# Kernel tuning notes

Hardware: AMD Instinct MI355X
Metric: run time of the kernel (lower is better)

The kernel has to match this reference:

```python
import jax, jax.numpy as jnp
import numpy as np
from functools import partial

H = 512          # hidden_size
H4 = H // 4      # goal hidden size
ENC = 8          # enc_steps
DEC = 12         # dec_steps
PRED = 2         # pred_dim (ETH)
B = 512          # batch


def _lin(k, i, o, s=0.05):
    kw, kb = jax.random.split(k)
    return jax.random.normal(kw, (i, o), jnp.float32) * s, jax.random.normal(kb, (o,), jnp.float32) * s


def setup_inputs() -> dict:
    key = jax.random.key(0)
    ks = jax.random.split(key, 32)
    d = {"inputs": jax.random.normal(ks[0], (B, ENC, 6), jnp.float32)}
    d["embed_w"], d["embed_b"] = _lin(ks[1], 6, H)
    d["reg_w"], d["reg_b"] = _lin(ks[2], H, PRED)
    d["ea_w"], d["ea_b"] = _lin(ks[3], H4, 1)
    d["da_w"], d["da_b"] = _lin(ks[4], H4, 1)
    d["e2g_w"], d["e2g_b"] = _lin(ks[5], H, H4)
    d["e2d_w"], d["e2d_b"] = _lin(ks[6], H, H)
    d["gh2i_w"], d["gh2i_b"] = _lin(ks[7], H4, H4)
    d["dh2i_w"], d["dh2i_b"] = _lin(ks[8], H, H)
    d["gh2t_w"], d["gh2t_b"] = _lin(ks[9], H4, H)
    d["g2e_w"], d["g2e_b"] = _lin(ks[10], H4, H4)
    d["g2d_w"], d["g2d_b"] = _lin(ks[11], H4, H4)
    d["enc_wih"], _ = _lin(ks[12], H + H4, 3 * H)
    d["enc_whh"], _ = _lin(ks[13], H, 3 * H)
    d["enc_bih"] = jax.random.normal(ks[14], (3 * H,), jnp.float32) * 0.05
    d["enc_bhh"] = jax.random.normal(ks[15], (3 * H,), jnp.float32) * 0.05
    d["goal_wih"], _ = _lin(ks[16], H4, 3 * H4)
    d["goal_whh"], _ = _lin(ks[17], H4, 3 * H4)
    d["goal_bih"] = jax.random.normal(ks[18], (3 * H4,), jnp.float32) * 0.05
    d["goal_bhh"] = jax.random.normal(ks[19], (3 * H4,), jnp.float32) * 0.05
    d["dec_wih"], _ = _lin(ks[20], H + H4, 3 * H)
    d["dec_whh"], _ = _lin(ks[21], H, 3 * H)
    d["dec_bih"] = jax.random.normal(ks[22], (3 * H,), jnp.float32) * 0.05
    d["dec_bhh"] = jax.random.normal(ks[23], (3 * H,), jnp.float32) * 0.05
    return d


def _gru(x, h, wih, whh, bih, bhh):
    gi = x @ wih + bih          # [B, 3H]
    gh = h @ whh + bhh
    ir, iz, inn = jnp.split(gi, 3, axis=-1)
    hr, hz, hn = jnp.split(gh, 3, axis=-1)
    r = jax.nn.sigmoid(ir + hr)
    z = jax.nn.sigmoid(iz + hz)
    n = jnp.tanh(inn + r * hn)
    return (1.0 - z) * n + z * h


def reference(inputs, embed_w, embed_b, reg_w, reg_b, ea_w, ea_b, da_w, da_b,
              e2g_w, e2g_b, e2d_w, e2d_b, gh2i_w, gh2i_b, dh2i_w, dh2i_b,
              gh2t_w, gh2t_b, g2e_w, g2e_b, g2d_w, g2d_b,
              enc_wih, enc_whh, enc_bih, enc_bhh,
              goal_wih, goal_whh, goal_bih, goal_bhh,
              dec_wih, dec_whh, dec_bih, dec_bhh):
    relu = jax.nn.relu
    b = inputs.shape[0]
    traj_input = relu(inputs @ embed_w + embed_b)           # [B, ENC, H]

    def sge(goal_hidden):
        def gstep(carry, _):
            gh, gi = carry
            gh = _gru(gi, gh, goal_wih, goal_whh, goal_bih, goal_bhh)
            gi = relu(gh @ gh2i_w + gh2i_b)
            return (gh, gi), gh
        gi0 = jnp.zeros((b, H4), traj_input.dtype)
        _, goals = jax.lax.scan(gstep, (goal_hidden, gi0), None, length=DEC)  # [DEC,B,H4]
        goal_traj = relu(goals @ gh2t_w + gh2t_b) @ reg_w + reg_b             # [DEC,B,PRED]
        goal_for_dec = relu(goals @ g2d_w + g2d_b)                            # [DEC,B,H4]
        gfe = relu(goals @ g2e_w + g2e_b).transpose(1, 0, 2)                  # [B,DEC,H4]
        logits = relu(jnp.tanh(gfe) @ ea_w + ea_b)[..., 0]                    # [B,DEC]
        attn = jax.nn.softmax(logits, axis=1)
        goal_for_enc = jnp.einsum('bt,bth->bh', attn, gfe)
        return goal_for_dec, goal_for_enc, goal_traj.transpose(1, 0, 2)

    def decoder(dec_hidden, gfd):
        gfd_b = gfd.transpose(1, 0, 2)  # [B,DEC,H4]
        steps = jnp.arange(DEC)
        def dstep(dh, t):
            mask = (steps >= t)[None, :, None]
            gdi = jnp.where(mask, gfd_b, 0.0)                      # zeros before t, faithful to torch
            logits = relu(jnp.tanh(gdi) @ da_w + da_b)[..., 0]     # [B,DEC]
            attn = jax.nn.softmax(logits, axis=1)
            ctx = jnp.einsum('bt,bth->bh', attn, gdi)
            ddi = relu(dh @ dh2i_w + dh2i_b)
            x = jnp.concatenate([ctx, ddi], axis=-1)
            dh = _gru(x, dh, dec_wih, dec_whh, dec_bih, dec_bhh)
            return dh, dh @ reg_w + reg_b
        _, traj = jax.lax.scan(dstep, dec_hidden, steps)           # [DEC,B,PRED]
        return traj.transpose(1, 0, 2)

    def estep(carry, x_t):
        teh, gfe = carry
        teh = _gru(jnp.concatenate([x_t, gfe], axis=1), teh,
                   enc_wih, enc_whh, enc_bih, enc_bhh)
        goal_hidden = relu(teh @ e2g_w + e2g_b)
        dec_hidden = relu(teh @ e2d_w + e2d_b)
        gfd, gfe, goal_traj = sge(goal_hidden)
        dec_traj = decoder(dec_hidden, gfd)
        return (teh, gfe), (goal_traj, dec_traj)

    teh0 = jnp.zeros((b, H), traj_input.dtype)
    gfe0 = jnp.zeros((b, H4), traj_input.dtype)
    _, (all_goal, all_dec) = jax.lax.scan(estep, (teh0, gfe0),
                                          traj_input.transpose(1, 0, 2))
    # [ENC,B,DEC,PRED] -> [B,ENC,DEC,PRED]
    return all_goal.transpose(1, 0, 2, 3), all_dec.transpose(1, 0, 2, 3)
```

## Files before the change

kernel.cpp:

```cpp
#include <hip/hip_runtime.h>


typedef unsigned short u16;
typedef __attribute__((ext_vector_type(8))) short bf16x8;
typedef __attribute__((ext_vector_type(4))) float f32x4;

static __device__ __forceinline__ float b2f(u16 u) {
  union { float f; unsigned int i; } x; x.i = ((unsigned int)u) << 16; return x.f;
}
static __device__ __forceinline__ u16 f2b(float f) {
  unsigned int u = __float_as_uint(f);
  unsigned int r = (u + 0x7FFFu + ((u >> 16) & 1u)) >> 16;
  return (u16)r;
}
static __device__ __forceinline__ float fsig(float x) {
  return __fdividef(1.f, 1.f + __expf(-x));
}
static __device__ __forceinline__ float ftanh(float x) {
  return 1.f - __fdividef(2.f, __expf(2.f * x) + 1.f);
}

struct TransArgs {
  const float* in[13];
  u16* out[13];
  int K[13], N[13], t0[13], nx[13];
};

__global__ __launch_bounds__(256) void transpose_all(TransArgs ta) {
  int bid = blockIdx.x;
  int i = 0;
  for (int k = 1; k < 13; k++) if (bid >= ta.t0[k]) i = k;
  const float* in = ta.in[i];
  u16* out = ta.out[i];
  int K = ta.K[i], N = ta.N[i];
  int local = bid - ta.t0[i];
  int nx = ta.nx[i];
  int tx = local % nx, ty = local / nx;
  __shared__ u16 tbuf[32][33];
  int n0 = tx * 32, k0 = ty * 32;
  int x = threadIdx.x & 31, y = threadIdx.x >> 5;
  for (int q = 0; q < 4; q++) tbuf[y + 8 * q][x] = f2b(in[(size_t)(k0 + y + 8 * q) * N + n0 + x]);
  __syncthreads();
  for (int q = 0; q < 4; q++) out[(size_t)(n0 + y + 8 * q) * K + k0 + x] = tbuf[x][y + 8 * q];
}

__global__ __launch_bounds__(256) void embed_kernel(const float* __restrict__ inp,
                                                    const float* __restrict__ w,
                                                    const float* __restrict__ bias,
                                                    u16* __restrict__ traj) {
  int t = blockIdx.x * 256 + threadIdx.x;
  int h = t & 511, b = (t >> 9) & 511, e = t >> 18;
  float acc = bias[h];
  for (int i = 0; i < 6; i++) acc += inp[(b * 8 + e) * 6 + i] * w[i * 512 + h];
  traj[((e * 512) + b) * 512 + h] = f2b(fmaxf(acc, 0.f));
}

struct GDesc {
  const u16* A; int lda;
  const u16* A2; int lda2; int asplit;
  const u16* W; int ldw;
  const float* bias;
  u16* Cb; int ldc;
  float* Cf;
  u16* Cb2; int ldc2; int route_n;
  int K; int relu; int nblk;
};

__global__ __launch_bounds__(256) void gemm128(GDesc d0, GDesc d1) {
  GDesc d = (blockIdx.z == 0) ? d0 : d1;
  if ((int)blockIdx.x >= d.nblk) return;
  __shared__ u16 As[128][72];
  __shared__ u16 Bs[128][72];
  int tid = threadIdx.x;
  int m0 = blockIdx.y * 128, n0 = blockIdx.x * 128;
  int lane = tid & 63, wave = tid >> 6;
  int wr = wave >> 1, wc = wave & 1;
  int mrow = lane & 15, kq = (lane >> 4) * 8;
  int srow = tid >> 3, scol = (tid & 7) * 8;
  f32x4 acc[4][4] = {};

  for (int k0 = 0; k0 < d.K; k0 += 64) {
    const u16* Asrc; int Alda, kk;
    if (k0 < d.asplit) { Asrc = d.A; Alda = d.lda; kk = k0; }
    else               { Asrc = d.A2; Alda = d.lda2; kk = k0 - d.asplit; }
    __syncthreads();
#pragma unroll
    for (int p = 0; p < 4; p++) {
      int r = srow + p * 32;
      *(uint4*)&As[r][scol] = *(const uint4*)&Asrc[(size_t)(m0 + r) * Alda + kk + scol];
      *(uint4*)&Bs[r][scol] = *(const uint4*)&d.W[(size_t)(n0 + r) * d.ldw + k0 + scol];
    }
    __syncthreads();
#pragma unroll
    for (int ks = 0; ks < 2; ks++) {
      bf16x8 af[4], bf[4];
#pragma unroll
      for (int i = 0; i < 4; i++) {
        af[i] = *(const bf16x8*)&As[wr * 64 + i * 16 + mrow][ks * 32 + kq];
        bf[i] = *(const bf16x8*)&Bs[wc * 64 + i * 16 + mrow][ks * 32 + kq];
      }
#pragma unroll
      for (int i = 0; i < 4; i++)
#pragma unroll
        for (int j = 0; j < 4; j++)
          acc[i][j] = __builtin_amdgcn_mfma_f32_16x16x32_bf16(af[i], bf[j], acc[i][j], 0, 0, 0);
    }
  }
  int col = lane & 15, rq = (lane >> 4) * 4;
#pragma unroll
  for (int j = 0; j < 4; j++) {
    int n = n0 + wc * 64 + j * 16 + col;
    float bv = d.bias ? d.bias[n] : 0.f;
    bool r2 = (n >= d.route_n);
    u16* cb = r2 ? d.Cb2 : d.Cb;
    int ldc = r2 ? d.ldc2 : d.ldc;
    int nn = r2 ? n - d.route_n : n;
#pragma unroll
    for (int i = 0; i < 4; i++)
#pragma unroll
      for (int r = 0; r < 4; r++) {
        int m = m0 + wr * 64 + i * 16 + rq + r;
        float v = acc[i][j][r] + bv;
        if (d.relu) v = fmaxf(v, 0.f);
        cb[(size_t)m * ldc + nn] = f2b(v);
        if (d.Cf) d.Cf[(size_t)m * d.ldc + n] = v;
      }
  }
}

__global__ __launch_bounds__(256) void gru_pw_reg(const u16* __restrict__ gi,
                                                  const u16* __restrict__ gh,
                                                  float* __restrict__ hf,
                                                  u16* __restrict__ hb,
                                                  const float* __restrict__ rw,
                                                  const float* __restrict__ rb,
                                                  float* __restrict__ out, int td) {
  int t = blockIdx.x * 256 + threadIdx.x;
  int r = t >> 6, lane = threadIdx.x & 63;
  int j8 = lane * 8;
  size_t base = (size_t)r * 1536 + j8;
  uint4 ir4 = *(const uint4*)&gi[base];
  uint4 iz4 = *(const uint4*)&gi[base + 512];
  uint4 in4 = *(const uint4*)&gi[base + 1024];
  uint4 hr4 = *(const uint4*)&gh[base];
  uint4 hz4 = *(const uint4*)&gh[base + 512];
  uint4 hn4 = *(const uint4*)&gh[base + 1024];
  const u16* irp = (const u16*)&ir4; const u16* izp = (const u16*)&iz4;
  const u16* inp = (const u16*)&in4; const u16* hrp = (const u16*)&hr4;
  const u16* hzp = (const u16*)&hz4; const u16* hnp = (const u16*)&hn4;
  size_t hoff = (size_t)r * 512 + j8;
  float hv[8];
  *(float4*)&hv[0] = *(const float4*)&hf[hoff];
  *(float4*)&hv[4] = *(const float4*)&hf[hoff + 4];
  u16 hbv[8];
  float p0 = 0.f, p1 = 0.f;
  for (int j = 0; j < 8; j++) {
    float rr = fsig(b2f(irp[j]) + b2f(hrp[j]));
    float zz = fsig(b2f(izp[j]) + b2f(hzp[j]));
    float nn = ftanh(b2f(inp[j]) + rr * b2f(hnp[j]));
    float ho = (1.f - zz) * nn + zz * hv[j];
    hv[j] = ho; hbv[j] = f2b(ho);
    p0 += ho * rw[(j8 + j) * 2];
    p1 += ho * rw[(j8 + j) * 2 + 1];
  }
  *(float4*)&hf[hoff] = *(const float4*)&hv[0];
  *(float4*)&hf[hoff + 4] = *(const float4*)&hv[4];
  *(uint4*)&hb[hoff] = *(const uint4*)&hbv[0];
  for (int o = 32; o; o >>= 1) { p0 += __shfl_down(p0, o); p1 += __shfl_down(p1, o); }
  if (lane == 0) {
    int e = r >> 9, b = r & 511;
    size_t off = ((size_t)(b * 8 + e) * 12 + td) * 2;
    out[off] = p0 + rb[0];
    out[off + 1] = p1 + rb[1];
  }
}

__global__ __launch_bounds__(1024) void goal_mega(const u16* __restrict__ gi_g,
                                                  const u16* __restrict__ gh_g,
                                                  float* __restrict__ teh_f,
                                                  u16* __restrict__ teh_out,
                                                  const u16* __restrict__ e2g_t,
                                                  const float* __restrict__ e2g_b,
                                                  const u16* __restrict__ wih_t,
                                                  const u16* __restrict__ whh_t,
                                                  const float* __restrict__ bih,
                                                  const float* __restrict__ bhh,
                                                  const u16* __restrict__ g2i_t,
                                                  const float* __restrict__ g2i_b,
                                                  const u16* __restrict__ g2e_t,
                                                  const float* __restrict__ g2e_b,
                                                  const float* __restrict__ eaw,
                                                  const float* __restrict__ eab,
                                                  u16* __restrict__ goals,
                                                  u16* __restrict__ gfe_out) {
  __shared__ float ghf[16][128];
  __shared__ u16   ghb[16][136];
  __shared__ u16   gib[16][136];
  __shared__ float gi3[16][388];
  __shared__ float gh3[16][388];
  __shared__ u16   gfe_l[12][16][128];
  __shared__ u16   tehb[16][520];
  int tid = threadIdx.x;
  int r0 = blockIdx.x * 16;
  int lane = tid & 63, wave = tid >> 6;
  int mrow = lane & 15, kq = (lane >> 4) * 8;
  int rq4 = (lane >> 4) * 4;

  bf16x8 Bf[3][4];
  float  bias1[3];
  int    n0s[3];
  bool   isIv[3];
#pragma unroll
  for (int i = 0; i < 3; i++) {
    int tt = wave + 16 * i;
    bool iI = tt < 24;
    int n0 = (iI ? tt : tt - 24) * 16;
    isIv[i] = iI; n0s[i] = n0;
    const u16* Wt = iI ? wih_t : whh_t;
#pragma unroll
    for (int ks = 0; ks < 4; ks++)
      Bf[i][ks] = *(const bf16x8*)&Wt[(n0 + mrow) * 128 + ks * 32 + kq];
    bias1[i] = (iI ? bih : bhh)[n0 + mrow];
  }
  bf16x8 Gf[4];
  float bias3;
  {
    const u16* W3 = (wave < 8) ? g2i_t : g2e_t;
    const float* B3 = (wave < 8) ? g2i_b : g2e_b;
    int n0 = (wave & 7) * 16;
#pragma unroll
    for (int ks = 0; ks < 4; ks++)
      Gf[ks] = *(const bf16x8*)&W3[(n0 + mrow) * 128 + ks * 32 + kq];
    bias3 = B3[n0 + mrow];
  }

  {
    u16* gz = &gib[0][0];
    for (int idx = tid; idx < 16 * 136; idx += 1024) gz[idx] = 0;
  }

  {
    int r = wave;
    int j8 = lane * 8;
    int grow = r0 + r;
    size_t base = (size_t)grow * 1536 + j8;
    uint4 ir4 = *(const uint4*)&gi_g[base];
    uint4 iz4 = *(const uint4*)&gi_g[base + 512];
    uint4 in4 = *(const uint4*)&gi_g[base + 1024];
    uint4 hr4 = *(const uint4*)&gh_g[base];
    uint4 hz4 = *(const uint4*)&gh_g[base + 512];
    uint4 hn4 = *(const uint4*)&gh_g[base + 1024];
    const u16* irp = (const u16*)&ir4; const u16* izp = (const u16*)&iz4;
    const u16* inp = (const u16*)&in4; const u16* hrp = (const u16*)&hr4;
    const u16* hzp = (const u16*)&hz4; const u16* hnp = (const u16*)&hn4;
    size_t hoff = (size_t)grow * 512 + j8;
    float hv[8];
    *(float4*)&hv[0] = *(const float4*)&teh_f[hoff];
    *(float4*)&hv[4] = *(const float4*)&teh_f[hoff + 4];
    u16 hbv[8];
    for (int j = 0; j < 8; j++) {
      float rr = fsig(b2f(irp[j]) + b2f(hrp[j]));
      float zz = fsig(b2f(izp[j]) + b2f(hzp[j]));
      float nn = ftanh(b2f(inp[j]) + rr * b2f(hnp[j]));
      float ho = (1.f - zz) * nn + zz * hv[j];
      hv[j] = ho; hbv[j] = f2b(ho);
    }
    *(float4*)&teh_f[hoff] = *(const float4*)&hv[0];
    *(float4*)&teh_f[hoff + 4] = *(const float4*)&hv[4];
    *(uint4*)&teh_out[hoff] = *(const uint4*)&hbv[0];
    *(uint4*)&tehb[r][j8] = *(const uint4*)&hbv[0];
  }
  __syncthreads();

  if (wave < 8) {
    int n0 = wave * 16;
    f32x4 acc = {};
#pragma unroll
    for (int ks = 0; ks < 16; ks++) {
      bf16x8 a = *(const bf16x8*)&tehb[mrow][ks * 32 + kq];
      bf16x8 b = *(const bf16x8*)&e2g_t[(size_t)(n0 + mrow) * 512 + ks * 32 + kq];
      acc = __builtin_amdgcn_mfma_f32_16x16x32_bf16(a, b, acc, 0, 0, 0);
    }
    int n = n0 + mrow;
    float bv = e2g_b[n];
#pragma unroll
    for (int r = 0; r < 4; r++) {
      float v = fmaxf(acc[r] + bv, 0.f);
      int m = rq4 + r;
      ghf[m][n] = v;
      ghb[m][n] = f2b(v);
    }
  }
  __syncthreads();

  for (int t = 0; t < 12; t++) {
    bf16x8 agi[4], agh[4];
#pragma unroll
    for (int ks = 0; ks < 4; ks++) {
      agi[ks] = *(const bf16x8*)&gib[mrow][ks * 32 + kq];
      agh[ks] = *(const bf16x8*)&ghb[mrow][ks * 32 + kq];
    }
#pragma unroll
    for (int i = 0; i < 3; i++) {
      f32x4 acc = {};
#pragma unroll
      for (int ks = 0; ks < 4; ks++)
        acc = __builtin_amdgcn_mfma_f32_16x16x32_bf16(isIv[i] ? agi[ks] : agh[ks],
                                                      Bf[i][ks], acc, 0, 0, 0);
      float* G = isIv[i] ? &gi3[0][0] : &gh3[0][0];
      int n = n0s[i] + mrow;
#pragma unroll
      for (int r = 0; r < 4; r++)
        G[(rq4 + r) * 388 + n] = acc[r] + bias1[i];
    }
    __syncthreads();
    for (int idx = tid; idx < 2048; idx += 1024) {
      int m = idx >> 7, j = idx & 127;
      float rr = fsig(gi3[m][j] + gh3[m][j]);
      float zz = fsig(gi3[m][128 + j] + gh3[m][128 + j]);
      float nn = ftanh(gi3[m][256 + j] + rr * gh3[m][256 + j]);
      float h = ghf[m][j];
      float ho = (1.f - zz) * nn + zz * h;
      ghf[m][j] = ho;
      u16 hb = f2b(ho);
      ghb[m][j] = hb;
      goals[(t * 512 + r0 + m) * 128 + j] = hb;
    }
    __syncthreads();
    {
      f32x4 acc = {};
#pragma unroll
      for (int ks = 0; ks < 4; ks++) {
        bf16x8 a = *(const bf16x8*)&ghb[mrow][ks * 32 + kq];
        acc = __builtin_amdgcn_mfma_f32_16x16x32_bf16(a, Gf[ks], acc, 0, 0, 0);
      }
      int n = (wave & 7) * 16 + mrow;
      if (wave < 8) {
#pragma unroll
        for (int r = 0; r < 4; r++)
          gib[rq4 + r][n] = f2b(fmaxf(acc[r] + bias3, 0.f));
      } else {
#pragma unroll
        for (int r = 0; r < 4; r++)
          gfe_l[t][rq4 + r][n] = f2b(fmaxf(acc[r] + bias3, 0.f));
      }
    }
    __syncthreads();
  }

  {
    int m = wave;
    float w0 = eaw[lane], w1 = eaw[lane + 64];
    float eb = eab[0];
    float v0[12], v1[12], lg[12];
#pragma unroll
    for (int t = 0; t < 12; t++) {
      float a = b2f(gfe_l[t][m][lane]);
      float c = b2f(gfe_l[t][m][lane + 64]);
      v0[t] = a; v1[t] = c;
      float p = ftanh(a) * w0 + ftanh(c) * w1;
      for (int o = 32; o; o >>= 1) p += __shfl_xor(p, o);
      lg[t] = fmaxf(p + eb, 0.f);
    }
    float mx = lg[0];
#pragma unroll
    for (int t = 1; t < 12; t++) mx = fmaxf(mx, lg[t]);
    float s = 0.f;
#pragma unroll
    for (int t = 0; t < 12; t++) { lg[t] = __expf(lg[t] - mx); s += lg[t]; }
    float inv = __fdividef(1.f, s);
    float c0 = 0.f, c1 = 0.f;
#pragma unroll
    for (int t = 0; t < 12; t++) { c0 += lg[t] * inv * v0[t]; c1 += lg[t] * inv * v1[t]; }
    gfe_out[(r0 + m) * 128 + lane] = f2b(c0);
    gfe_out[(r0 + m) * 128 + lane + 64] = f2b(c1);
  }
}

__global__ __launch_bounds__(256) void regdot_goal(const u16* __restrict__ X,
                                                   const float* __restrict__ rw,
                                                   const float* __restrict__ rb,
                                                   float* __restrict__ out) {
  int row = (blockIdx.x * 256 + threadIdx.x) >> 6;
  int lane = threadIdx.x & 63;
  int k0 = lane * 8;
  uint4 xv = *(const uint4*)&X[(size_t)row * 512 + k0];
  const u16* xp = (const u16*)&xv;
  float p0 = 0.f, p1 = 0.f;
  for (int j = 0; j < 8; j++) {
    float x = b2f(xp[j]);
    p0 += x * rw[(k0 + j) * 2];
    p1 += x * rw[(k0 + j) * 2 + 1];
  }
  for (int o = 32; o; o >>= 1) { p0 += __shfl_down(p0, o); p1 += __shfl_down(p1, o); }
  if (lane == 0) {
    int s = row >> 9, b = row & 511;
    int e = s / 12, td = s - e * 12;
    size_t off = ((size_t)(b * 8 + e) * 12 + td) * 2;
    out[off] = p0 + rb[0];
    out[off + 1] = p1 + rb[1];
  }
}

__global__ __launch_bounds__(256) void attn_ctx_all(const u16* __restrict__ gfd,
                                                    const float* __restrict__ daw,
                                                    const float* __restrict__ dab,
                                                    u16* __restrict__ xctx) {
  __shared__ u16 rowbuf[1536];
  int row = blockIdx.x;
  int tid = threadIdx.x;
  int e = row >> 9, b = row & 511;
  for (int idx = tid; idx < 1536; idx += 256) {
    int s = idx >> 7, h = idx & 127;
    rowbuf[idx] = gfd[((size_t)(e * 12 + s) * 512 + b) * 128 + h];
  }
  __syncthreads();
  int lane = tid & 63, wave = tid >> 6;
  float w0 = daw[lane], w1 = daw[lane + 64];
  float bias = dab[0];
  float base = fmaxf(bias, 0.f);
  for (int q = 0; q < 3; q++) {
    int td = wave + q * 4;
    float v0[12], v1[12], lg[12];
    for (int s = 0; s < 12; s++) {
      if (s < td) { lg[s] = base; v0[s] = 0.f; v1[s] = 0.f; }
      else {
        float a = b2f(rowbuf[s * 128 + lane]);
        float c = b2f(rowbuf[s * 128 + 64 + lane]);
        v0[s] = a; v1[s] = c;
        float p = ftanh(a) * w0 + ftanh(c) * w1;
        for (int o = 32; o; o >>= 1) p += __shfl_xor(p, o);
        lg[s] = fmaxf(p + bias, 0.f);
      }
    }
    float m = lg[0];
    for (int s = 1; s < 12; s++) m = fmaxf(m, lg[s]);
    float ssum = 0.f;
    for (int s = 0; s < 12; s++) { lg[s] = __expf(lg[s] - m); ssum += lg[s]; }
    float inv = __fdividef(1.f, ssum);
    float c0 = 0.f, c1 = 0.f;
    for (int s = 0; s < 12; s++) { c0 += lg[s] * inv * v0[s]; c1 += lg[s] * inv * v1[s]; }
    size_t o = ((size_t)td * 4096 + row) * 128;
    xctx[o + lane] = f2b(c0);
    xctx[o + lane + 64] = f2b(c1);
  }
}

extern "C" void kernel_launch(void* const* d_in, const int* in_sizes, int n_in,
                              void* d_out, int out_size, void* d_ws, size_t ws_size,
                              hipStream_t stream) {
  const float* inp      = (const float*)d_in[0];
  const float* embed_w  = (const float*)d_in[1];
  const float* embed_b  = (const float*)d_in[2];
  const float* reg_w    = (const float*)d_in[3];
  const float* reg_b    = (const float*)d_in[4];
  const float* ea_w     = (const float*)d_in[5];
  const float* ea_b     = (const float*)d_in[6];
  const float* da_w     = (const float*)d_in[7];
  const float* da_b     = (const float*)d_in[8];
  const float* e2g_w    = (const float*)d_in[9];
  const float* e2g_b    = (const float*)d_in[10];
  const float* e2d_w    = (const float*)d_in[11];
  const float* e2d_b    = (const float*)d_in[12];
  const float* gh2i_w   = (const float*)d_in[13];
  const float* gh2i_b   = (const float*)d_in[14];
  const float* dh2i_w   = (const float*)d_in[15];
  const float* dh2i_b   = (const float*)d_in[16];
  const float* gh2t_w   = (const float*)d_in[17];
  const float* gh2t_b   = (const float*)d_in[18];
  const float* g2e_w    = (const float*)d_in[19];
  const float* g2e_b    = (const float*)d_in[20];
  const float* g2d_w    = (const float*)d_in[21];
  const float* g2d_b    = (const float*)d_in[22];
  const float* enc_wih  = (const float*)d_in[23];
  const float* enc_whh  = (const float*)d_in[24];
  const float* enc_bih  = (const float*)d_in[25];
  const float* enc_bhh  = (const float*)d_in[26];
  const float* goal_wih = (const float*)d_in[27];
  const float* goal_whh = (const float*)d_in[28];
  const float* goal_bih = (const float*)d_in[29];
  const float* goal_bhh = (const float*)d_in[30];
  const float* dec_wih  = (const float*)d_in[31];
  const float* dec_whh  = (const float*)d_in[32];
  const float* dec_bih  = (const float*)d_in[33];
  const float* dec_bhh  = (const float*)d_in[34];

  char* ws = (char*)d_ws;
  size_t off = 0;
  auto alloc = [&](size_t bytes) -> char* {
    char* p = ws + off; off += (bytes + 255) & ~(size_t)255; return p;
  };
  const size_t TSZ = 512 * 512;
  float* teh_f    = (float*)alloc(TSZ * 4);
  u16*   teh_hist = (u16*)  alloc(9 * TSZ * 2);
  u16*   gfe_buf  = (u16*)  alloc(512 * 128 * 2);
  size_t zero_bytes = off;
  u16*   traj     = (u16*)  alloc((size_t)8 * TSZ * 2);
  u16*   goals_all= (u16*)  alloc((size_t)8 * 6144 * 128 * 2);
  u16*   ghid     = (u16*)  alloc((size_t)49152 * 512 * 2);
  u16*   gfd      = (u16*)  alloc((size_t)49152 * 128 * 2);
  u16*   xctx     = (u16*)  alloc((size_t)12 * 4096 * 128 * 2);
  float* dh_f     = (float*)alloc((size_t)4096 * 512 * 4);
  u16*   dh_b     = (u16*)  alloc((size_t)4096 * 512 * 2);
  u16*   ddi      = (u16*)  alloc((size_t)4096 * 512 * 2);
  u16*   giD      = (u16*)  alloc((size_t)4096 * 1536 * 2);
  u16*   ghD      = (u16*)  alloc((size_t)4096 * 1536 * 2);
  u16*   giE = giD, *ghE = ghD;
  u16* enc_wih_t  = (u16*)alloc((size_t)1536 * 640 * 2);
  u16* enc_whh_t  = (u16*)alloc((size_t)1536 * 512 * 2);
  u16* dec_wih_t  = (u16*)alloc((size_t)1536 * 640 * 2);
  u16* dec_whh_t  = (u16*)alloc((size_t)1536 * 512 * 2);
  u16* e2g_t      = (u16*)alloc(128 * 512 * 2);
  u16* e2d_t      = (u16*)alloc(512 * 512 * 2);
  u16* dh2i_t     = (u16*)alloc(512 * 512 * 2);
  u16* head_t     = (u16*)alloc(640 * 128 * 2);
  u16* g2e_t      = (u16*)alloc(128 * 128 * 2);
  u16* goal_wih_t = (u16*)alloc(384 * 128 * 2);
  u16* goal_whh_t = (u16*)alloc(384 * 128 * 2);
  u16* gh2i_t     = (u16*)alloc(128 * 128 * 2);
  float* head_b   = (float*)alloc(640 * 4);
  if (off > ws_size) return;

  float* out_goal = (float*)d_out;
  float* out_dec  = out_goal + (size_t)512 * 8 * 12 * 2;

  hipMemsetAsync(teh_f, 0, zero_bytes, stream);

  TransArgs ta;
  int ntile = 0, ti = 0;
  auto push = [&](const float* in, u16* out, int K, int N) {
    ta.in[ti] = in; ta.out[ti] = out; ta.K[ti] = K; ta.N[ti] = N;
    ta.t0[ti] = ntile; ta.nx[ti] = N / 32;
    ntile += (K / 32) * (N / 32); ti++;
  };
  push(enc_wih, enc_wih_t, 640, 1536);
  push(enc_whh, enc_whh_t, 512, 1536);
  push(dec_wih, dec_wih_t, 640, 1536);
  push(dec_whh, dec_whh_t, 512, 1536);
  push(e2g_w, e2g_t, 512, 128);
  push(e2d_w, e2d_t, 512, 512);
  push(dh2i_w, dh2i_t, 512, 512);
  push(gh2t_w, head_t, 128, 512);
  push(g2d_w, head_t + 512 * 128, 128, 128);
  push(g2e_w, g2e_t, 128, 128);
  push(goal_wih, goal_wih_t, 128, 384);
  push(goal_whh, goal_whh_t, 128, 384);
  push(gh2i_w, gh2i_t, 128, 128);
  transpose_all<<<ntile, 256, 0, stream>>>(ta);
  hipMemcpyAsync(head_b, gh2t_b, 512 * 4, hipMemcpyDeviceToDevice, stream);
  hipMemcpyAsync(head_b + 512, g2d_b, 128 * 4, hipMemcpyDeviceToDevice, stream);

  embed_kernel<<<8192, 256, 0, stream>>>(inp, embed_w, embed_b, traj);

  const int FAR = 1 << 30;

  for (int e = 0; e < 8; ++e) {
    GDesc dgi{traj + (size_t)e * TSZ, 512, gfe_buf, 128, 512,
              enc_wih_t, 640, enc_bih, giE, 1536, nullptr,
              nullptr, 0, FAR, 640, 0, 12};
    GDesc dgh{teh_hist + (size_t)e * TSZ, 512, nullptr, 0, FAR,
              enc_whh_t, 512, enc_bhh, ghE, 1536, nullptr,
              nullptr, 0, FAR, 512, 0, 12};
    gemm128<<<dim3(12, 4, 2), 256, 0, stream>>>(dgi, dgh);
    goal_mega<<<32, 1024, 0, stream>>>(giE, ghE, teh_f, teh_hist + (size_t)(e + 1) * TSZ,
                                       e2g_t, e2g_b,
                                       goal_wih_t, goal_whh_t, goal_bih, goal_bhh,
                                       gh2i_t, gh2i_b, g2e_t, g2e_b, ea_w, ea_b,
                                       goals_all + (size_t)e * 6144 * 128, gfe_buf);
  }

  {
    GDesc de2d{teh_hist + TSZ, 512, nullptr, 0, FAR,
               e2d_t, 512, e2d_b, dh_b, 512, dh_f,
               nullptr, 0, FAR, 512, 1, 4};
    gemm128<<<dim3(4, 32, 1), 256, 0, stream>>>(de2d, de2d);
    GDesc dhead{goals_all, 128, nullptr, 0, FAR,
                head_t, 128, head_b, ghid, 512, nullptr,
                gfd, 128, 512, 128, 1, 5};
    gemm128<<<dim3(5, 384, 1), 256, 0, stream>>>(dhead, dhead);
    regdot_goal<<<12288, 256, 0, stream>>>(ghid, reg_w, reg_b, out_goal);
    attn_ctx_all<<<4096, 256, 0, stream>>>(gfd, da_w, da_b, xctx);
  }

  for (int td = 0; td < 12; ++td) {
    GDesc dd1{dh_b, 512, nullptr, 0, FAR,
              dh2i_t, 512, dh2i_b, ddi, 512, nullptr,
              nullptr, 0, FAR, 512, 1, 4};
    GDesc dd2{dh_b, 512, nullptr, 0, FAR,
              dec_whh_t, 512, dec_bhh, ghD, 1536, nullptr,
              nullptr, 0, FAR, 512, 0, 12};
    gemm128<<<dim3(12, 32, 2), 256, 0, stream>>>(dd1, dd2);
    GDesc dgi{xctx + (size_t)td * 4096 * 128, 128, ddi, 512, 128,
              dec_wih_t, 640, dec_bih, giD, 1536, nullptr,
              nullptr, 0, FAR, 640, 0, 12};
    gemm128<<<dim3(12, 32, 1), 256, 0, stream>>>(dgi, dgi);
    gru_pw_reg<<<1024, 256, 0, stream>>>(giD, ghD, dh_f, dh_b, reg_w, reg_b, out_dec, td);
  }
}
```

Before: 1.356 ms.

## Fuse goal regression into head GEMM, dh2i into GRU pointwise, restructure attention

The goal-head GEMM now does the reg_w projection in its epilogue, using shuffles and atomicAdd into a pre-zeroed output, so the large ghid intermediate is never written. In the decoder loop, the dh2i projection for the next step moves into the GRU pointwise kernel as a per-block MFMA over the fresh hidden state. This lets gi and gh run in one merged GEMM launch per step instead of two dependent launches. attn_ctx_all now computes all 12 masked softmax contexts with a suffix-sum recurrence in one pass per wave. The cost is atomics, with float summation order that is no longer deterministic, plus a small, poorly parallel GEMM inside the pointwise kernel.

```diff
diff --git a/kernel.cpp b/kernel.cpp
--- a/kernel.cpp
+++ b/kernel.cpp
@@ -63,12 +63,13 @@
   u16* Cb; int ldc;
   float* Cf;
   u16* Cb2; int ldc2; int route_n;
-  int K; int relu; int nblk;
+  int K; int relu; int nblk; int mblk;
+  const float* regw; const float* regb; float* regout;
 };
 
 __global__ __launch_bounds__(256) void gemm128(GDesc d0, GDesc d1) {
   GDesc d = (blockIdx.z == 0) ? d0 : d1;
-  if ((int)blockIdx.x >= d.nblk) return;
+  if ((int)blockIdx.x >= d.nblk || (int)blockIdx.y >= d.mblk) return;
   __shared__ u16 As[128][72];
   __shared__ u16 Bs[128][72];
   int tid = threadIdx.x;
@@ -107,6 +108,48 @@
     }
   }
   int col = lane & 15, rq = (lane >> 4) * 4;
+  bool isreg = (d.regout != nullptr) && (n0 < d.route_n);
+  if (isreg) {
+    float pr0[4][4] = {}, pr1[4][4] = {};
+#pragma unroll
+    for (int j = 0; j < 4; j++) {
+      int n = n0 + wc * 64 + j * 16 + col;
+      float bv = d.bias ? d.bias[n] : 0.f;
+      float rw0 = d.regw[n * 2], rw1 = d.regw[n * 2 + 1];
+#pragma unroll
+      for (int i = 0; i < 4; i++)
+#pragma unroll
+        for (int r = 0; r < 4; r++) {
+          float v = fmaxf(acc[i][j][r] + bv, 0.f);
+          pr0[i][r] += v * rw0;
+          pr1[i][r] += v * rw1;
+        }
+    }
+#pragma unroll
+    for (int i = 0; i < 4; i++)
+#pragma unroll
+      for (int r = 0; r < 4; r++)
+#pragma unroll
+        for (int o = 1; o < 16; o <<= 1) {
+          pr0[i][r] += __shfl_xor(pr0[i][r], o);
+          pr1[i][r] += __shfl_xor(pr1[i][r], o);
+        }
+    if (col == 0) {
+      bool addb = (blockIdx.x == 0 && wc == 0);
+#pragma unroll
+      for (int i = 0; i < 4; i++)
+#pragma unroll
+        for (int r = 0; r < 4; r++) {
+          int m = m0 + wr * 64 + i * 16 + rq + r;
+          int ee = m / 6144; int rem = m - ee * 6144;
+          int t = rem >> 9; int b = rem & 511;
+          float* o = d.regout + ((size_t)(b * 8 + ee) * 12 + t) * 2;
+          atomicAdd(o, pr0[i][r] + (addb ? d.regb[0] : 0.f));
+          atomicAdd(o + 1, pr1[i][r] + (addb ? d.regb[1] : 0.f));
+        }
+    }
+    return;
+  }
 #pragma unroll
   for (int j = 0; j < 4; j++) {
     int n = n0 + wc * 64 + j * 16 + col;
@@ -128,51 +171,81 @@
   }
 }
 
-__global__ __launch_bounds__(256) void gru_pw_reg(const u16* __restrict__ gi,
-                                                  const u16* __restrict__ gh,
-                                                  float* __restrict__ hf,
-                                                  u16* __restrict__ hb,
-                                                  const float* __restrict__ rw,
-                                                  const float* __restrict__ rb,
-                                                  float* __restrict__ out, int td) {
-  int t = blockIdx.x * 256 + threadIdx.x;
-  int r = t >> 6, lane = threadIdx.x & 63;
-  int j8 = lane * 8;
-  size_t base = (size_t)r * 1536 + j8;
-  uint4 ir4 = *(const uint4*)&gi[base];
-  uint4 iz4 = *(const uint4*)&gi[base + 512];
-  uint4 in4 = *(const uint4*)&gi[base + 1024];
-  uint4 hr4 = *(const uint4*)&gh[base];
-  uint4 hz4 = *(const uint4*)&gh[base + 512];
-  uint4 hn4 = *(const uint4*)&gh[base + 1024];
-  const u16* irp = (const u16*)&ir4; const u16* izp = (const u16*)&iz4;
-  const u16* inp = (const u16*)&in4; const u16* hrp = (const u16*)&hr4;
-  const u16* hzp = (const u16*)&hz4; const u16* hnp = (const u16*)&hn4;
-  size_t hoff = (size_t)r * 512 + j8;
-  float hv[8];
-  *(float4*)&hv[0] = *(const float4*)&hf[hoff];
-  *(float4*)&hv[4] = *(const float4*)&hf[hoff + 4];
-  u16 hbv[8];
-  float p0 = 0.f, p1 = 0.f;
-  for (int j = 0; j < 8; j++) {
-    float rr = fsig(b2f(irp[j]) + b2f(hrp[j]));
-    float zz = fsig(b2f(izp[j]) + b2f(hzp[j]));
-    float nn = ftanh(b2f(inp[j]) + rr * b2f(hnp[j]));
-    float ho = (1.f - zz) * nn + zz * hv[j];
-    hv[j] = ho; hbv[j] = f2b(ho);
-    p0 += ho * rw[(j8 + j) * 2];
-    p1 += ho * rw[(j8 + j) * 2 + 1];
-  }
-  *(float4*)&hf[hoff] = *(const float4*)&hv[0];
-  *(float4*)&hf[hoff + 4] = *(const float4*)&hv[4];
-  *(uint4*)&hb[hoff] = *(const uint4*)&hbv[0];
-  for (int o = 32; o; o >>= 1) { p0 += __shfl_down(p0, o); p1 += __shfl_down(p1, o); }
-  if (lane == 0) {
-    int e = r >> 9, b = r & 511;
-    size_t off = ((size_t)(b * 8 + e) * 12 + td) * 2;
-    out[off] = p0 + rb[0];
-    out[off + 1] = p1 + rb[1];
-  }
+__global__ __launch_bounds__(1024) void gru_dh2i_reg(const u16* __restrict__ gi,
+                                                     const u16* __restrict__ gh,
+                                                     float* __restrict__ hf,
+                                                     u16* __restrict__ hb,
+                                                     const u16* __restrict__ w_t,
+                                                     const float* __restrict__ wb,
+                                                     u16* __restrict__ ddi,
+                                                     const float* __restrict__ rw,
+                                                     const float* __restrict__ rb,
+                                                     float* __restrict__ out, int td) {
+  __shared__ u16 dhs[16][520];
+  __shared__ u16 dds[16][520];
+  int tid = threadIdx.x;
+  int lane = tid & 63, wave = tid >> 6;
+  int r0 = blockIdx.x * 16;
+  {
+    int r = r0 + wave;
+    int j8 = lane * 8;
+    size_t base = (size_t)r * 1536 + j8;
+    uint4 ir4 = *(const uint4*)&gi[base];
+    uint4 iz4 = *(const uint4*)&gi[base + 512];
+    uint4 in4 = *(const uint4*)&gi[base + 1024];
+    uint4 hr4 = *(const uint4*)&gh[base];
+    uint4 hz4 = *(const uint4*)&gh[base + 512];
+    uint4 hn4 = *(const uint4*)&gh[base + 1024];
+    const u16* irp = (const u16*)&ir4; const u16* izp = (const u16*)&iz4;
+    const u16* inp = (const u16*)&in4; const u16* hrp = (const u16*)&hr4;
+    const u16* hzp = (const u16*)&hz4; const u16* hnp = (const u16*)&hn4;
+    size_t hoff = (size_t)r * 512 + j8;
+    float hv[8];
+    *(float4*)&hv[0] = *(const float4*)&hf[hoff];
+    *(float4*)&hv[4] = *(const float4*)&hf[hoff + 4];
+    u16 hbv[8];
+    float p0 = 0.f, p1 = 0.f;
+    for (int j = 0; j < 8; j++) {
+      float rr = fsig(b2f(irp[j]) + b2f(hrp[j]));
+      float zz = fsig(b2f(izp[j]) + b2f(hzp[j]));
+      float nn = ftanh(b2f(inp[j]) + rr * b2f(hnp[j]));
+      float ho = (1.f - zz) * nn + zz * hv[j];
+      hv[j] = ho; hbv[j] = f2b(ho);
+      p0 += ho * rw[(j8 + j) * 2];
+      p1 += ho * rw[(j8 + j) * 2 + 1];
+    }
+    *(float4*)&hf[hoff] = *(const float4*)&hv[0];
+    *(float4*)&hf[hoff + 4] = *(const float4*)&hv[4];
+    *(uint4*)&hb[hoff] = *(const uint4*)&hbv[0];
+    *(uint4*)&dhs[wave][j8] = *(const uint4*)&hbv[0];
+    for (int o = 32; o; o >>= 1) { p0 += __shfl_down(p0, o); p1 += __shfl_down(p1, o); }
+    if (lane == 0) {
+      int e = r >> 9, b = r & 511;
+      size_t off = ((size_t)(b * 8 + e) * 12 + td) * 2;
+      out[off] = p0 + rb[0];
+      out[off + 1] = p1 + rb[1];
+    }
+  }
+  __syncthreads();
+  int mrow = lane & 15, kq = (lane >> 4) * 8, rq4 = (lane >> 4) * 4;
+#pragma unroll
+  for (int q = 0; q < 2; q++) {
+    int n0 = (wave * 2 + q) * 16;
+    f32x4 acc = {};
+#pragma unroll
+    for (int ks = 0; ks < 16; ks++) {
+      bf16x8 a = *(const bf16x8*)&dhs[mrow][ks * 32 + kq];
+      bf16x8 bfr = *(const bf16x8*)&w_t[(size_t)(n0 + mrow) * 512 + ks * 32 + kq];
+      acc = __builtin_amdgcn_mfma_f32_16x16x32_bf16(a, bfr, acc, 0, 0, 0);
+    }
+    float bv = wb[n0 + mrow];
+#pragma unroll
+    for (int x = 0; x < 4; x++)
+      dds[rq4 + x][n0 + mrow] = f2b(fmaxf(acc[x] + bv, 0.f));
+  }
+  __syncthreads();
+  int rr = tid >> 6, c8 = (tid & 63) * 8;
+  *(uint4*)&ddi[(size_t)(r0 + rr) * 512 + c8] = *(const uint4*)&dds[rr][c8];
 }
 
 __global__ __launch_bounds__(1024) void goal_mega(const u16* __restrict__ gi_g,
@@ -377,72 +450,44 @@
   }
 }
 
-__global__ __launch_bounds__(256) void regdot_goal(const u16* __restrict__ X,
-                                                   const float* __restrict__ rw,
-                                                   const float* __restrict__ rb,
-                                                   float* __restrict__ out) {
-  int row = (blockIdx.x * 256 + threadIdx.x) >> 6;
-  int lane = threadIdx.x & 63;
-  int k0 = lane * 8;
-  uint4 xv = *(const uint4*)&X[(size_t)row * 512 + k0];
-  const u16* xp = (const u16*)&xv;
-  float p0 = 0.f, p1 = 0.f;
-  for (int j = 0; j < 8; j++) {
-    float x = b2f(xp[j]);
-    p0 += x * rw[(k0 + j) * 2];
-    p1 += x * rw[(k0 + j) * 2 + 1];
-  }
-  for (int o = 32; o; o >>= 1) { p0 += __shfl_down(p0, o); p1 += __shfl_down(p1, o); }
-  if (lane == 0) {
-    int s = row >> 9, b = row & 511;
-    int e = s / 12, td = s - e * 12;
-    size_t off = ((size_t)(b * 8 + e) * 12 + td) * 2;
-    out[off] = p0 + rb[0];
-    out[off + 1] = p1 + rb[1];
-  }
-}
-
 __global__ __launch_bounds__(256) void attn_ctx_all(const u16* __restrict__ gfd,
                                                     const float* __restrict__ daw,
                                                     const float* __restrict__ dab,
                                                     u16* __restrict__ xctx) {
-  __shared__ u16 rowbuf[1536];
-  int row = blockIdx.x;
-  int tid = threadIdx.x;
+  int row = (blockIdx.x * 256 + threadIdx.x) >> 6;
+  int lane = threadIdx.x & 63;
   int e = row >> 9, b = row & 511;
-  for (int idx = tid; idx < 1536; idx += 256) {
-    int s = idx >> 7, h = idx & 127;
-    rowbuf[idx] = gfd[((size_t)(e * 12 + s) * 512 + b) * 128 + h];
-  }
-  __syncthreads();
-  int lane = tid & 63, wave = tid >> 6;
   float w0 = daw[lane], w1 = daw[lane + 64];
   float bias = dab[0];
+  float v0[12], v1[12], lg[12];
+#pragma unroll
+  for (int s = 0; s < 12; s++) {
+    size_t o = ((size_t)(e * 12 + s) * 512 + b) * 128;
+    float a = b2f(gfd[o + lane]);
+    float c = b2f(gfd[o + 64 + lane]);
+    v0[s] = a; v1[s] = c;
+    float p = ftanh(a) * w0 + ftanh(c) * w1;
+    for (int o2 = 32; o2; o2 >>= 1) p += __shfl_xor(p, o2);
+    lg[s] = fmaxf(p + bias, 0.f);
+  }
   float base = fmaxf(bias, 0.f);
-  for (int q = 0; q < 3; q++) {
-    int td = wave + q * 4;
-    float v0[12], v1[12], lg[12];
-    for (int s = 0; s < 12; s++) {
-      if (s < td) { lg[s] = base; v0[s] = 0.f; v1[s] = 0.f; }
-      else {
-        float a = b2f(rowbuf[s * 128 + lane]);
-        float c = b2f(rowbuf[s * 128 + 64 + lane]);
-        v0[s] = a; v1[s] = c;
-        float p = ftanh(a) * w0 + ftanh(c) * w1;
-        for (int o = 32; o; o >>= 1) p += __shfl_xor(p, o);
-        lg[s] = fmaxf(p + bias, 0.f);
-      }
-    }
-    float m = lg[0];
-    for (int s = 1; s < 12; s++) m = fmaxf(m, lg[s]);
-    float ssum = 0.f;
-    for (int s = 0; s < 12; s++) { lg[s] = __expf(lg[s] - m); ssum += lg[s]; }
-    float inv = __fdividef(1.f, ssum);
-    float c0 = 0.f, c1 = 0.f;
-    for (int s = 0; s < 12; s++) { c0 += lg[s] * inv * v0[s]; c1 += lg[s] * inv * v1[s]; }
+  float m = base;
+#pragma unroll
+  for (int s = 0; s < 12; s++) m = fmaxf(m, lg[s]);
+  float eb = __expf(base - m);
+  float el[12];
+#pragma unroll
+  for (int s = 0; s < 12; s++) el[s] = __expf(lg[s] - m);
+  float S0 = 0.f, S1 = 0.f, sufE = 0.f;
+#pragma unroll
+  for (int td = 11; td >= 0; td--) {
+    sufE += el[td];
+    S0 += el[td] * v0[td];
+    S1 += el[td] * v1[td];
+    float inv = __fdividef(1.f, (float)td * eb + sufE);
     size_t o = ((size_t)td * 4096 + row) * 128;
-    xctx[o + lane] = f2b(c0);
-    xctx[o + lane + 64] = f2b(c1);
+    xctx[o + lane] = f2b(S0 * inv);
+    xctx[o + lane + 64] = f2b(S1 * inv);
   }
 }
 
@@ -497,7 +542,6 @@
   size_t zero_bytes = off;
   u16*   traj     = (u16*)  alloc((size_t)8 * TSZ * 2);
   u16*   goals_all= (u16*)  alloc((size_t)8 * 6144 * 128 * 2);
-  u16*   ghid     = (u16*)  alloc((size_t)49152 * 512 * 2);
   u16*   gfd      = (u16*)  alloc((size_t)49152 * 128 * 2);
   u16*   xctx     = (u16*)  alloc((size_t)12 * 4096 * 128 * 2);
   float* dh_f     = (float*)alloc((size_t)4096 * 512 * 4);
@@ -525,6 +569,7 @@
   float* out_dec  = out_goal + (size_t)512 * 8 * 12 * 2;
 
   hipMemsetAsync(teh_f, 0, zero_bytes, stream);
+  hipMemsetAsync(out_goal, 0, (size_t)512 * 8 * 12 * 2 * 4, stream);
 
   TransArgs ta;
   int ntile = 0, ti = 0;
@@ -557,10 +602,10 @@
   for (int e = 0; e < 8; ++e) {
     GDesc dgi{traj + (size_t)e * TSZ, 512, gfe_buf, 128, 512,
               enc_wih_t, 640, enc_bih, giE, 1536, nullptr,
-              nullptr, 0, FAR, 640, 0, 12};
+              nullptr, 0, FAR, 640, 0, 12, 4, nullptr, nullptr, nullptr};
     GDesc dgh{teh_hist + (size_t)e * TSZ, 512, nullptr, 0, FAR,
               enc_whh_t, 512, enc_bhh, ghE, 1536, nullptr,
-              nullptr, 0, FAR, 512, 0, 12};
+              nullptr, 0, FAR, 512, 0, 12, 4, nullptr, nullptr, nullptr};
     gemm128<<<dim3(12, 4, 2), 256, 0, stream>>>(dgi, dgh);
     goal_mega<<<32, 1024, 0, stream>>>(giE, ghE, teh_f, teh_hist + (size_t)(e + 1) * TSZ,
                                        e2g_t, e2g_b,
@@ -570,30 +615,29 @@
   }
 
   {
+    GDesc dhead{goals_all, 128, nullptr, 0, FAR,
+                head_t, 128, head_b, nullptr, 512, nullptr,
+                gfd, 128, 512, 128, 1, 5, 384, reg_w, reg_b, out_goal};
     GDesc de2d{teh_hist + TSZ, 512, nullptr, 0, FAR,
                e2d_t, 512, e2d_b, dh_b, 512, dh_f,
-               nullptr, 0, FAR, 512, 1, 4};
-    gemm128<<<dim3(4, 32, 1), 256, 0, stream>>>(de2d, de2d);
-    GDesc dhead{goals_all, 128, nullptr, 0, FAR,
-                head_t, 128, head_b, ghid, 512, nullptr,
-                gfd, 128, 512, 128, 1, 5};
-    gemm128<<<dim3(5, 384, 1), 256, 0, stream>>>(dhead, dhead);
-    regdot_goal<<<12288, 256, 0, stream>>>(ghid, reg_w, reg_b, out_goal);
-    attn_ctx_all<<<4096, 256, 0, stream>>>(gfd, da_w, da_b, xctx);
+               nullptr, 0, FAR, 512, 1, 4, 32, nullptr, nullptr, nullptr};
+    gemm128<<<dim3(5, 384, 2), 256, 0, stream>>>(dhead, de2d);
+    attn_ctx_all<<<1024, 256, 0, stream>>>(gfd, da_w, da_b, xctx);
+    GDesc dd0{dh_b, 512, nullptr, 0, FAR,
+              dh2i_t, 512, dh2i_b, ddi, 512, nullptr,
+              nullptr, 0, FAR, 512, 1, 4, 32, nullptr, nullptr, nullptr};
+    gemm128<<<dim3(4, 32, 1), 256, 0, stream>>>(dd0, dd0);
   }
 
   for (int td = 0; td < 12; ++td) {
-    GDesc dd1{dh_b, 512, nullptr, 0, FAR,
-              dh2i_t, 512, dh2i_b, ddi, 512, nullptr,
-              nullptr, 0, FAR, 512, 1, 4};
-    GDesc dd2{dh_b, 512, nullptr, 0, FAR,
-              dec_whh_t, 512, dec_bhh, ghD, 1536, nullptr,
-              nullptr, 0, FAR, 512, 0, 12};
-    gemm128<<<dim3(12, 32, 2), 256, 0, stream>>>(dd1, dd2);
     GDesc dgi{xctx + (size_t)td * 4096 * 128, 128, ddi, 512, 128,
               dec_wih_t, 640, dec_bih, giD, 1536, nullptr,
-              nullptr, 0, FAR, 640, 0, 12};
-    gemm128<<<dim3(12, 32, 1), 256, 0, stream>>>(dgi, dgi);
-    gru_pw_reg<<<1024, 256, 0, stream>>>(giD, ghD, dh_f, dh_b, reg_w, reg_b, out_dec, td);
-  }
-}
+              nullptr, 0, FAR, 640, 0, 12, 32, nullptr, nullptr, nullptr};
+    GDesc dgh{dh_b, 512, nullptr, 0, FAR,
+              dec_whh_t, 512, dec_bhh, ghD, 1536, nullptr,
+              nullptr, 0, FAR, 512, 0, 12, 32, nullptr, nullptr, nullptr};
+    gemm128<<<dim3(12, 32, 2), 256, 0, stream>>>(dgi, dgh);
+    gru_dh2i_reg<<<256, 1024, 0, stream>>>(giD, ghD, dh_f, dh_b, dh2i_t, dh2i_b, ddi,
+                                           reg_w, reg_b, out_dec, td);
+  }
+}
```

Result: slower. 1.461 ms (+7.8%).
